# Kernel tuning notes

Hardware: AMD Instinct MI355X
Metric: run time of the kernel (lower is better)

## Reference

```python
import jax, jax.numpy as jnp
import numpy as np

EPS = 1e-5


def _bn_linear(x, g, b, W, c, relu):
    # BatchNorm1d over flattened (B*N) axis with batch statistics (training mode),
    # then Linear, then optional ReLU. x: [B, N, Din]
    mean = jnp.mean(x, axis=(0, 1))
    var = jnp.mean(jnp.square(x - mean), axis=(0, 1))  # biased variance, as torch BN uses in fwd
    xn = (x - mean) * jax.lax.rsqrt(var + EPS) * g + b
    y = jnp.einsum('bnd,od->bno', xn, W) + c
    return jax.nn.relu(y) if relu else y


def setup_inputs() -> dict:
    key = jax.random.key(0)
    ks = jax.random.split(key, 8)
    B, N = 32, 2048
    dims = [256, 512, 512, 1024]  # in_size, hidden_sizes..., out_size
    inp = {"set_feats": jax.random.normal(ks[0], (B, N, dims[0]), dtype=jnp.float32)}
    for i, (din, dout) in enumerate(zip(dims[:-1], dims[1:])):
        inp[f"g{i}"] = jnp.ones((din,), jnp.float32)
        inp[f"b{i}"] = jnp.zeros((din,), jnp.float32)
        inp[f"W{i}"] = jax.random.normal(ks[1 + i], (dout, din), dtype=jnp.float32) / np.sqrt(din)
        inp[f"c{i}"] = jax.random.normal(ks[4 + i], (dout,), dtype=jnp.float32) * 0.01
    return inp


def reference(set_feats, g0, b0, W0, c0, g1, b1, W1, c1, g2, b2, W2, c2):
    x = _bn_linear(set_feats, g0, b0, W0, c0, relu=True)
    x = _bn_linear(x, g1, b1, W1, c1, relu=True)
    x = _bn_linear(x, g2, b2, W2, c2, relu=False)
    # reduction = 'max' over the set dimension (-2)
    return jnp.max(x, axis=-2)
```

## Files before the change

kernel.cpp:

```cpp
#include <hip/hip_runtime.h>
#include <hip/hip_bf16.h>
#include <stdint.h>

typedef unsigned short u16;
typedef __attribute__((ext_vector_type(8))) __bf16 bf16x8;
typedef __attribute__((ext_vector_type(4))) float f32x4;

#define BN_EPS 1e-5f
#define MROWS 65536
#define INV_M (1.0f / 65536.0f)
#define NREP 16

__device__ __forceinline__ u16 f2bf(float f) {
  unsigned u = __builtin_bit_cast(unsigned, f);
  unsigned r = (u + 0x7FFFu + ((u >> 16) & 1u)) >> 16;
  return (u16)r;
}
__device__ __forceinline__ float bf2f(u16 h) {
  return __builtin_bit_cast(float, (unsigned)h << 16);
}

__global__ __launch_bounds__(256)
void stats_cast_k(const float* __restrict__ x, u16* __restrict__ xbf,
                  float* __restrict__ srep ) {
  const int t = threadIdx.x;
  const int tc = t & 63, tr = t >> 6;
  const int rb = blockIdx.x * 32 + tr * 8;
  float4 v[8];
#pragma unroll
  for (int i = 0; i < 8; ++i)
    v[i] = *(const float4*)(x + (size_t)(rb + i) * 256 + tc * 4);
  float s0 = 0, s1 = 0, s2 = 0, s3 = 0, q0 = 0, q1 = 0, q2 = 0, q3 = 0;
#pragma unroll
  for (int i = 0; i < 8; ++i) {
    ushort4 ov;
    ov.x = f2bf(v[i].x); ov.y = f2bf(v[i].y);
    ov.z = f2bf(v[i].z); ov.w = f2bf(v[i].w);
    *(ushort4*)(xbf + (size_t)(rb + i) * 256 + tc * 4) = ov;
    s0 += v[i].x; q0 += v[i].x * v[i].x;
    s1 += v[i].y; q1 += v[i].y * v[i].y;
    s2 += v[i].z; q2 += v[i].z * v[i].z;
    s3 += v[i].w; q3 += v[i].w * v[i].w;
  }
  __shared__ float red[4][256];
  red[tr][tc * 4 + 0] = s0; red[tr][tc * 4 + 1] = s1;
  red[tr][tc * 4 + 2] = s2; red[tr][tc * 4 + 3] = s3;
  __syncthreads();
  float* dst = srep + (blockIdx.x & (NREP - 1)) * 512;
  if (tr == 0) {
#pragma unroll
    for (int i = 0; i < 4; ++i) {
      int c = tc * 4 + i;
      atomicAdd(&dst[c], red[0][c] + red[1][c] + red[2][c] + red[3][c]);
    }
  }
  __syncthreads();
  red[tr][tc * 4 + 0] = q0; red[tr][tc * 4 + 1] = q1;
  red[tr][tc * 4 + 2] = q2; red[tr][tc * 4 + 3] = q3;
  __syncthreads();
  if (tr == 0) {
#pragma unroll
    for (int i = 0; i < 4; ++i) {
      int c = tc * 4 + i;
      atomicAdd(&dst[256 + c], red[0][c] + red[1][c] + red[2][c] + red[3][c]);
    }
  }
}

__global__ __launch_bounds__(256)
void prep_w_k(const float* __restrict__ W, const float* __restrict__ g,
              const float* __restrict__ b, const float* __restrict__ c,
              const float* __restrict__ ssum, const float* __restrict__ ssq,
              int rep_stride, int nrep,
              u16* __restrict__ Wp, float* __restrict__ cp, int din, int dout) {
  const int gw = (blockIdx.x * 256 + threadIdx.x) >> 6;
  const int l = threadIdx.x & 63;
  if (gw >= dout) return;
  const int o = gw;
  float acc = 0.f;
  for (int d0 = l * 4; d0 < din; d0 += 256) {
    float sm[4] = {}, sq[4] = {};
    for (int r = 0; r < nrep; ++r) {
      float4 a = *(const float4*)(ssum + (size_t)r * rep_stride + d0);
      float4 z = *(const float4*)(ssq + (size_t)r * rep_stride + d0);
      sm[0] += a.x; sm[1] += a.y; sm[2] += a.z; sm[3] += a.w;
      sq[0] += z.x; sq[1] += z.y; sq[2] += z.z; sq[3] += z.w;
    }
    float4 wv = *(const float4*)(W + (size_t)o * din + d0);
    float4 gv = *(const float4*)(g + d0);
    float4 bv = *(const float4*)(b + d0);
    float w4[4] = {wv.x, wv.y, wv.z, wv.w};
    float g4[4] = {gv.x, gv.y, gv.z, gv.w};
    float b4[4] = {bv.x, bv.y, bv.z, bv.w};
    ushort4 ov;
    u16 o4[4];
#pragma unroll
    for (int i = 0; i < 4; ++i) {
      float mean = sm[i] * INV_M;
      float var = sq[i] * INV_M - mean * mean;
      float alpha = g4[i] * rsqrtf(var + BN_EPS);
      float beta = b4[i] - mean * alpha;
      o4[i] = f2bf(w4[i] * alpha);
      acc += w4[i] * beta;
    }
    ov.x = o4[0]; ov.y = o4[1]; ov.z = o4[2]; ov.w = o4[3];
    *(ushort4*)(Wp + (size_t)o * din + d0) = ov;
  }
#pragma unroll
  for (int off = 32; off > 0; off >>= 1) acc += __shfl_xor(acc, off, 64);
  if (l == 0) cp[o] = c[o] + acc;
}

#define GLDS16(gp, lp) __builtin_amdgcn_global_load_lds( \
    (__attribute__((address_space(1))) void*)(void*)(gp), \
    (__attribute__((address_space(3))) void*)(lp), 16, 0, 0)

template <bool RELU, bool DOMAX>
__global__ __launch_bounds__(512, 2)
void gemm_k(const u16* __restrict__ A, const u16* __restrict__ B,
            const float* __restrict__ cp, u16* __restrict__ Y,
            float* __restrict__ osum, float* __restrict__ osq,
            unsigned* __restrict__ maxbuf, int K, int N) {
  __shared__ __align__(16) u16 lds[8 * 8192];
  const int t = threadIdx.x;
  const int w = t >> 6, l = t & 63;
  const int lr = l & 15, lk = l >> 4;
  const int wm = w >> 2, wn = w & 3;

  const int cpx = (int)gridDim.x >> 3;
  int bid = (int)blockIdx.x;
  bid = (bid & 7) * cpx + (bid >> 3);
  const int tiles_n = N >> 8;
  const int tm0 = (bid / tiles_n) << 8;
  const int tn0 = (bid % tiles_n) << 8;

  const int srow = t >> 2;
  const int scol = (((t & 3) ^ ((t >> 3) & 3)) << 3);
  const u16* Ag = A + (size_t)(tm0 + srow) * K + scol;
  const u16* Bg = B + (size_t)(tn0 + srow) * K + scol;
  u16* const ldsA = lds;
  u16* const ldsB = lds + 4 * 8192;

#define STAGE_A(slot_, kt_) do { \
    GLDS16(Ag + (kt_) * 32, ldsA + (slot_) * 8192 + t * 8); \
    GLDS16(Ag + (size_t)128 * K + (kt_) * 32, ldsA + (slot_) * 8192 + 4096 + t * 8); \
  } while (0)
#define STAGE_B(slot_, kt_) do { \
    GLDS16(Bg + (kt_) * 32, ldsB + (slot_) * 8192 + t * 8); \
    GLDS16(Bg + (size_t)128 * K + (kt_) * 32, ldsB + (slot_) * 8192 + 4096 + t * 8); \
  } while (0)

  const int pc = (lk ^ ((lr >> 1) & 3)) * 8;
  const int rba = wm * 128 + lr;
  const int rbb = wn * 64 + lr;

  f32x4 acc[8][4] = {};
  const int nk = K >> 5;

  STAGE_A(0, 0); STAGE_B(0, 0);
  STAGE_A(1, 1); STAGE_B(1, 1);
  STAGE_A(2, 2); STAGE_B(2, 2);
  asm volatile("s_waitcnt vmcnt(8)" ::: "memory");
  __builtin_amdgcn_s_barrier();

  for (int T = 0; T < nk; ++T) {
    const int sl = T & 3;
    const u16* la = ldsA + sl * 8192;
    const u16* lb = ldsB + sl * 8192;
    bf16x8 af[4], bf[4];
#pragma unroll
    for (int n = 0; n < 4; ++n)
      bf[n] = *(const bf16x8*)(lb + (rbb + n * 16) * 32 + pc);
#pragma unroll
    for (int j = 0; j < 4; ++j)
      af[j] = *(const bf16x8*)(la + (rba + j * 16) * 32 + pc);
    if (T + 3 < nk) STAGE_A((T + 3) & 3, T + 3);
    __builtin_amdgcn_s_barrier();
    __builtin_amdgcn_s_setprio(1);
#pragma unroll
    for (int j = 0; j < 4; ++j)
#pragma unroll
      for (int n = 0; n < 4; ++n)
        acc[j][n] = __builtin_amdgcn_mfma_f32_16x16x32_bf16(af[j], bf[n], acc[j][n], 0, 0, 0);
    __builtin_amdgcn_s_setprio(0);
#pragma unroll
    for (int j = 0; j < 4; ++j)
      af[j] = *(const bf16x8*)(la + (rba + 64 + j * 16) * 32 + pc);
    if (T + 3 < nk) STAGE_B((T + 3) & 3, T + 3);
    if (T < nk - 3)       asm volatile("s_waitcnt vmcnt(8)" ::: "memory");
    else if (T == nk - 3) asm volatile("s_waitcnt vmcnt(4)" ::: "memory");
    else if (T == nk - 2) asm volatile("s_waitcnt vmcnt(0)" ::: "memory");
    __builtin_amdgcn_s_barrier();
    __builtin_amdgcn_s_setprio(1);
#pragma unroll
    for (int j = 0; j < 4; ++j)
#pragma unroll
      for (int n = 0; n < 4; ++n)
        acc[4 + j][n] = __builtin_amdgcn_mfma_f32_16x16x32_bf16(af[j], bf[n], acc[4 + j][n], 0, 0, 0);
    __builtin_amdgcn_s_setprio(0);
  }

  if (!DOMAX) {
    float cs[4] = {}, cq[4] = {};
#pragma unroll
    for (int n = 0; n < 4; ++n) {
      const int gcol = tn0 + wn * 64 + n * 16 + lr;
      const float cb = cp[gcol];
#pragma unroll
      for (int m = 0; m < 8; ++m) {
        const int grow = tm0 + wm * 128 + m * 16 + lk * 4;
#pragma unroll
        for (int r = 0; r < 4; ++r) {
          float v = acc[m][n][r] + cb;
          if (RELU) v = fmaxf(v, 0.f);
          Y[(size_t)(grow + r) * N + gcol] = f2bf(v);
          cs[n] += v;
          cq[n] += v * v;
        }
      }
    }
    if (RELU) {
#pragma unroll
      for (int n = 0; n < 4; ++n) {
        cs[n] += __shfl_xor(cs[n], 16, 64);
        cs[n] += __shfl_xor(cs[n], 32, 64);
        cq[n] += __shfl_xor(cq[n], 16, 64);
        cq[n] += __shfl_xor(cq[n], 32, 64);
      }
      float* sred = (float*)lds;
      __syncthreads();
      if (lk == 0) {
#pragma unroll
        for (int n = 0; n < 4; ++n) {
          const int c = wn * 64 + n * 16 + lr;
          sred[wm * 256 + c] = cs[n];
          sred[512 + wm * 256 + c] = cq[n];
        }
      }
      __syncthreads();
      if (t < 256) {
        atomicAdd(&osum[tn0 + t], sred[t] + sred[256 + t]);
      } else {
        const int c = t - 256;
        atomicAdd(&osq[tn0 + c], sred[512 + c] + sred[768 + c]);
      }
    }
  } else {
    const int batch = tm0 >> 11;
#pragma unroll
    for (int n = 0; n < 4; ++n) {
      const int gcol = tn0 + wn * 64 + n * 16 + lr;
      const float cb = cp[gcol];
      float mx = -3.0e38f;
#pragma unroll
      for (int m = 0; m < 8; ++m)
#pragma unroll
        for (int r = 0; r < 4; ++r)
          mx = fmaxf(mx, acc[m][n][r] + cb);
      mx = fmaxf(mx, __shfl_xor(mx, 16, 64));
      mx = fmaxf(mx, __shfl_xor(mx, 32, 64));
      if (lk == 0) {
        unsigned u = __builtin_bit_cast(unsigned, mx);
        u = (u & 0x80000000u) ? ~u : (u | 0x80000000u);
        atomicMax(&maxbuf[batch * N + gcol], u);
      }
    }
  }
#undef STAGE_A
#undef STAGE_B
}

__global__ void decode_k(const unsigned* __restrict__ mb, float* __restrict__ out, int n) {
  int i = blockIdx.x * 256 + threadIdx.x;
  if (i < n) {
    unsigned u = mb[i];
    u = (u & 0x80000000u) ? (u & 0x7FFFFFFFu) : ~u;
    out[i] = __builtin_bit_cast(float, u);
  }
}

extern "C" void kernel_launch(void* const* d_in, const int* in_sizes, int n_in,
                              void* d_out, int out_size, void* d_ws, size_t ws_size,
                              hipStream_t stream) {
  const float* x0 = (const float*)d_in[0];
  const float* g0 = (const float*)d_in[1];
  const float* b0 = (const float*)d_in[2];
  const float* W0 = (const float*)d_in[3];
  const float* c0 = (const float*)d_in[4];
  const float* g1 = (const float*)d_in[5];
  const float* b1 = (const float*)d_in[6];
  const float* W1 = (const float*)d_in[7];
  const float* c1 = (const float*)d_in[8];
  const float* g2 = (const float*)d_in[9];
  const float* b2 = (const float*)d_in[10];
  const float* W2 = (const float*)d_in[11];
  const float* c2 = (const float*)d_in[12];

  char* ws = (char*)d_ws;
  size_t off = 0;
  auto alloc = [&](size_t bytes) -> char* {
    char* p = ws + off;
    off += (bytes + 255) & ~(size_t)255;
    return p;
  };
  u16* x0bf = (u16*)alloc((size_t)MROWS * 256 * 2);
  u16* y1 = (u16*)alloc((size_t)MROWS * 512 * 2);
  u16* y2 = (u16*)alloc((size_t)MROWS * 512 * 2);
  float* s0rep = (float*)alloc((NREP * 512 + 1024 + 1024 + 32768) * 4);
  float* s1sum = s0rep + NREP * 512;
  float* s1sq = s1sum + 512;
  float* s2sum = s1sum + 1024;
  float* s2sq = s2sum + 512;
  unsigned* maxbuf = (unsigned*)(s1sum + 2048);
  const size_t zbytes = (size_t)(NREP * 512 + 2048 + 32768) * 4;
  u16* W0p = (u16*)alloc(512 * 256 * 2);
  u16* W1p = (u16*)alloc(512 * 512 * 2);
  u16* W2p = (u16*)alloc(1024 * 512 * 2);
  float* c0p = (float*)alloc(512 * 4);
  float* c1p = (float*)alloc(512 * 4);
  float* c2p = (float*)alloc(1024 * 4);
  if (off > ws_size) return;

  hipMemsetAsync(s0rep, 0, zbytes, stream);

  stats_cast_k<<<2048, 256, 0, stream>>>(x0, x0bf, s0rep);
  prep_w_k<<<128, 256, 0, stream>>>(W0, g0, b0, c0, s0rep, s0rep + 256, 512, NREP,
                                    W0p, c0p, 256, 512);
  gemm_k<true, false><<<512, 512, 0, stream>>>(x0bf, W0p, c0p, y1, s1sum, s1sq, nullptr, 256, 512);
  prep_w_k<<<128, 256, 0, stream>>>(W1, g1, b1, c1, s1sum, s1sq, 0, 1,
                                    W1p, c1p, 512, 512);
  gemm_k<true, false><<<512, 512, 0, stream>>>(y1, W1p, c1p, y2, s2sum, s2sq, nullptr, 512, 512);
  prep_w_k<<<256, 256, 0, stream>>>(W2, g2, b2, c2, s2sum, s2sq, 0, 1,
                                    W2p, c2p, 512, 1024);
  gemm_k<false, true><<<1024, 512, 0, stream>>>(y2, W2p, c2p, nullptr, nullptr, nullptr, maxbuf, 512, 1024);
  decode_k<<<128, 256, 0, stream>>>(maxbuf, (float*)d_out, 32768);
}
```

Before: 211.9 us.

## Load B fragments directly from global to registers, halve LDS footprint

```diff
diff --git a/kernel.cpp b/kernel.cpp
--- a/kernel.cpp
+++ b/kernel.cpp
@@ -121,7 +121,7 @@
             const float* __restrict__ cp, u16* __restrict__ Y,
             float* __restrict__ osum, float* __restrict__ osq,
             unsigned* __restrict__ maxbuf, int K, int N) {
-  __shared__ __align__(16) u16 lds[8 * 8192];
+  __shared__ __align__(16) u16 lds[4 * 8192];
   const int t = threadIdx.x;
   const int w = t >> 6, l = t & 63;
   const int lr = l & 15, lk = l >> 4;
@@ -137,68 +137,78 @@
   const int srow = t >> 2;
   const int scol = (((t & 3) ^ ((t >> 3) & 3)) << 3);
   const u16* Ag = A + (size_t)(tm0 + srow) * K + scol;
-  const u16* Bg = B + (size_t)(tn0 + srow) * K + scol;
   u16* const ldsA = lds;
-  u16* const ldsB = lds + 4 * 8192;
 
 #define STAGE_A(slot_, kt_) do { \
     GLDS16(Ag + (kt_) * 32, ldsA + (slot_) * 8192 + t * 8); \
     GLDS16(Ag + (size_t)128 * K + (kt_) * 32, ldsA + (slot_) * 8192 + 4096 + t * 8); \
   } while (0)
-#define STAGE_B(slot_, kt_) do { \
-    GLDS16(Bg + (kt_) * 32, ldsB + (slot_) * 8192 + t * 8); \
-    GLDS16(Bg + (size_t)128 * K + (kt_) * 32, ldsB + (slot_) * 8192 + 4096 + t * 8); \
-  } while (0)
+
+  const u16* Bc[4];
+#pragma unroll
+  for (int n = 0; n < 4; ++n)
+    Bc[n] = B + (size_t)(tn0 + wn * 64 + n * 16 + lr) * K + lk * 8;
+
+#define BLOAD(dst_, n_, kt_) \
+  asm volatile("global_load_dwordx4 %0, %1, off" \
+               : "=v"(dst_) : "v"(Bc[n_] + (size_t)(kt_) * 32) : "memory")
 
   const int pc = (lk ^ ((lr >> 1) & 3)) * 8;
   const int rba = wm * 128 + lr;
-  const int rbb = wn * 64 + lr;
 
   f32x4 acc[8][4] = {};
   const int nk = K >> 5;
 
-  STAGE_A(0, 0); STAGE_B(0, 0);
-  STAGE_A(1, 1); STAGE_B(1, 1);
-  STAGE_A(2, 2); STAGE_B(2, 2);
-  asm volatile("s_waitcnt vmcnt(8)" ::: "memory");
+  bf16x8 b0[4], b1[4];
+  BLOAD(b0[0], 0, 0); BLOAD(b0[1], 1, 0); BLOAD(b0[2], 2, 0); BLOAD(b0[3], 3, 0);
+  STAGE_A(0, 0); STAGE_A(1, 1); STAGE_A(2, 2);
+  asm volatile("s_waitcnt vmcnt(4)" ::: "memory");
+  __builtin_amdgcn_sched_barrier(0);
   __builtin_amdgcn_s_barrier();
 
-  for (int T = 0; T < nk; ++T) {
-    const int sl = T & 3;
-    const u16* la = ldsA + sl * 8192;
-    const u16* lb = ldsB + sl * 8192;
-    bf16x8 af[4], bf[4];
-#pragma unroll
-    for (int n = 0; n < 4; ++n)
-      bf[n] = *(const bf16x8*)(lb + (rbb + n * 16) * 32 + pc);
-#pragma unroll
-    for (int j = 0; j < 4; ++j)
-      af[j] = *(const bf16x8*)(la + (rba + j * 16) * 32 + pc);
-    if (T + 3 < nk) STAGE_A((T + 3) & 3, T + 3);
-    __builtin_amdgcn_s_barrier();
-    __builtin_amdgcn_s_setprio(1);
-#pragma unroll
-    for (int j = 0; j < 4; ++j)
-#pragma unroll
-      for (int n = 0; n < 4; ++n)
-        acc[j][n] = __builtin_amdgcn_mfma_f32_16x16x32_bf16(af[j], bf[n], acc[j][n], 0, 0, 0);
-    __builtin_amdgcn_s_setprio(0);
-#pragma unroll
-    for (int j = 0; j < 4; ++j)
-      af[j] = *(const bf16x8*)(la + (rba + 64 + j * 16) * 32 + pc);
-    if (T + 3 < nk) STAGE_B((T + 3) & 3, T + 3);
-    if (T < nk - 3)       asm volatile("s_waitcnt vmcnt(8)" ::: "memory");
-    else if (T == nk - 3) asm volatile("s_waitcnt vmcnt(4)" ::: "memory");
-    else if (T == nk - 2) asm volatile("s_waitcnt vmcnt(0)" ::: "memory");
-    __builtin_amdgcn_s_barrier();
-    __builtin_amdgcn_s_setprio(1);
-#pragma unroll
-    for (int j = 0; j < 4; ++j)
-#pragma unroll
-      for (int n = 0; n < 4; ++n)
-        acc[4 + j][n] = __builtin_amdgcn_mfma_f32_16x16x32_bf16(af[j], bf[n], acc[4 + j][n], 0, 0, 0);
-    __builtin_amdgcn_s_setprio(0);
-  }
+#define TILE_BODY(T_, bcur_, bnxt_) do { \
+    const int sl_ = (T_) & 3; \
+    const u16* la_ = ldsA + sl_ * 8192; \
+    if ((T_) + 1 < nk) { \
+      BLOAD(bnxt_[0], 0, (T_) + 1); BLOAD(bnxt_[1], 1, (T_) + 1); \
+      BLOAD(bnxt_[2], 2, (T_) + 1); BLOAD(bnxt_[3], 3, (T_) + 1); \
+    } \
+    bf16x8 af0_[4], af1_[4]; \
+    _Pragma("unroll") \
+    for (int j = 0; j < 4; ++j) \
+      af0_[j] = *(const bf16x8*)(la_ + (rba + j * 16) * 32 + pc); \
+    if ((T_) <= nk - 3)      asm volatile("s_waitcnt vmcnt(6)" ::: "memory"); \
+    else if ((T_) == nk - 2) asm volatile("s_waitcnt vmcnt(4)" ::: "memory"); \
+    else                     asm volatile("s_waitcnt vmcnt(0)" ::: "memory"); \
+    __builtin_amdgcn_sched_barrier(0); \
+    __builtin_amdgcn_s_barrier(); \
+    if ((T_) + 3 < nk) STAGE_A(((T_) + 3) & 3, (T_) + 3); \
+    __builtin_amdgcn_s_setprio(1); \
+    _Pragma("unroll") \
+    for (int j = 0; j < 4; ++j) \
+      _Pragma("unroll") \
+      for (int n = 0; n < 4; ++n) \
+        acc[j][n] = __builtin_amdgcn_mfma_f32_16x16x32_bf16(af0_[j], bcur_[n], acc[j][n], 0, 0, 0); \
+    __builtin_amdgcn_s_setprio(0); \
+    _Pragma("unroll") \
+    for (int j = 0; j < 4; ++j) \
+      af1_[j] = *(const bf16x8*)(la_ + (rba + 64 + j * 16) * 32 + pc); \
+    __builtin_amdgcn_s_setprio(1); \
+    _Pragma("unroll") \
+    for (int j = 0; j < 4; ++j) \
+      _Pragma("unroll") \
+      for (int n = 0; n < 4; ++n) \
+        acc[4 + j][n] = __builtin_amdgcn_mfma_f32_16x16x32_bf16(af1_[j], bcur_[n], acc[4 + j][n], 0, 0, 0); \
+    __builtin_amdgcn_s_setprio(0); \
+  } while (0)
+
+  for (int T = 0; T < nk; T += 2) {
+    TILE_BODY(T, b0, b1);
+    TILE_BODY(T + 1, b1, b0);
+  }
+#undef TILE_BODY
+#undef BLOAD
+#undef STAGE_A
 
   if (!DOMAX) {
     float cs[4] = {}, cq[4] = {};
@@ -266,8 +276,6 @@
       }
     }
   }
-#undef STAGE_A
-#undef STAGE_B
 }
 
 __global__ void decode_k(const unsigned* __restrict__ mb, float* __restrict__ out, int n) {
```

Result: slower. 240.4 us (+13.5%).
